# Optimization experiments

Measured on AMD Instinct MI355X. Metric: run time of the kernel, lower is better.

Reference implementation:

```python
import jax, jax.numpy as jnp
import numpy as np

NUM_FIELDS = 40
EMBED_DIM = 64
ATTN_DIM = 32

def _triu_index(n):
    i, j = np.triu_indices(n, k=1)
    return jnp.asarray(i, jnp.int32), jnp.asarray(j, jnp.int32)

def setup_inputs() -> dict:
    key = jax.random.key(0)
    k0, k1, k2, k3, k4, k5 = jax.random.split(key, 6)
    B = 8192
    inputs = jax.random.normal(k0, (B, NUM_FIELDS, EMBED_DIM), dtype=jnp.float32)
    # attention MLP params (PyTorch Linear default init scale ~ 1/sqrt(fan_in))
    s1 = 1.0 / np.sqrt(EMBED_DIM)
    s2 = 1.0 / np.sqrt(ATTN_DIM)
    W1 = jax.random.uniform(k1, (EMBED_DIM, ATTN_DIM), jnp.float32, -s1, s1)
    b1 = jax.random.uniform(k2, (ATTN_DIM,), jnp.float32, -s1, s1)
    w2 = jax.random.uniform(k3, (ATTN_DIM,), jnp.float32, -s2, s2)
    p = jax.random.uniform(k4, (EMBED_DIM,), jnp.float32, -s1, s1)
    return {"inputs": inputs, "W1": W1, "b1": b1, "w2": w2, "p": p}

def reference(inputs, W1, b1, w2, p):
    idx0, idx1 = _triu_index(NUM_FIELDS)  # [P], P = 780 pairs
    # gather pairwise field embeddings and take elementwise product: [B, P, D]
    prod = inputs[:, idx0, :] * inputs[:, idx1, :]
    # tiny attention MLP: Linear -> ReLU -> Linear(no bias) -> softmax over pairs
    h = jax.nn.relu(jnp.einsum('bpd,da->bpa', prod, W1) + b1)  # [B, P, A]
    logits = jnp.einsum('bpa,a->bp', h, w2)                    # [B, P]
    attn = jax.nn.softmax(logits, axis=1)                      # softmax over pair dim
    # attention-weighted sum pooling over pairs: [B, D]
    pooled = jnp.einsum('bp,bpd->bd', attn, prod)
    # final linear projection to scalar (dropout=0 / eval -> identity)
    return jnp.einsum('bd,d->b', pooled, p)
```

## Files before the change

kernel.cpp:

```cpp
#include <hip/hip_runtime.h>


typedef _Float16 f16;
typedef f16 f16x2 __attribute__((ext_vector_type(2)));
typedef f16 f16x8 __attribute__((ext_vector_type(8)));
typedef float fx16 __attribute__((ext_vector_type(16)));

#define NF 40
#define NB 8192

union V8 { f16x8 v8; f16x2 v2[4]; };

__global__ __launch_bounds__(256, 4) void afm_kernel(
    const float* __restrict__ x,
    const float* __restrict__ W1,
    const float* __restrict__ b1,
    const float* __restrict__ w2,
    const float* __restrict__ p,
    float* __restrict__ out)
{
    __shared__ f16 xh[4][NF * 64];

    const int wid  = threadIdx.x >> 6;
    const int lane = threadIdx.x & 63;
    const int b    = blockIdx.x * 4 + wid;
    f16* Xs = &xh[wid][0];

    const float4* xb = (const float4*)(x + (size_t)b * (NF * 64));
#pragma unroll
    for (int t = 0; t < 5; ++t) {
        int id = t * 64 + lane;
        float4 v0 = xb[id * 2];
        float4 v1 = xb[id * 2 + 1];
        f16x8 h = { (f16)v0.x, (f16)v0.y, (f16)v0.z, (f16)v0.w,
                    (f16)v1.x, (f16)v1.y, (f16)v1.z, (f16)v1.w };
        int row = id >> 3, g = id & 7;
        int blk = g ^ (row & 7);
        *(f16x8*)(Xs + (row << 6) + blk * 8) = h;
    }
    __syncthreads();

    const int nl = lane & 31;
    const int hh = lane >> 5;
    const int h8 = hh * 8;

    f16x8 w1f[4];
#pragma unroll
    for (int kt = 0; kt < 4; ++kt)
#pragma unroll
        for (int j = 0; j < 8; ++j)
            w1f[kt][j] = (f16)W1[(kt * 16 + h8 + j) * 32 + nl];

    f16x2 pp[16];
#pragma unroll
    for (int kt = 0; kt < 4; ++kt)
#pragma unroll
        for (int m = 0; m < 4; ++m) {
            f16x2 t2 = { (f16)p[kt * 16 + h8 + 2 * m], (f16)p[kt * 16 + h8 + 2 * m + 1] };
            pp[kt * 4 + m] = t2;
        }

    fx16 b1C;
    float w2v[16];
#pragma unroll
    for (int r = 0; r < 16; ++r) {
        int a = (r & 3) + 8 * (r >> 2) + 4 * hh;
        b1C[r] = b1[a];
        w2v[r] = w2[a];
    }

    f16x8 xif[4];
    {
        int rb = nl & 7;
        const f16* rowp = Xs + (nl << 6);
#pragma unroll
        for (int kt = 0; kt < 4; ++kt) {
            int blk = (kt * 2 + hh) ^ rb;
            xif[kt] = *(const f16x8*)(rowp + blk * 8);
        }
    }

    float accW = 0.f, accWS = 0.f;

    auto body = [&](const f16x8* xi, int jrow, bool masked, bool valid) {
        int rb = jrow & 7;
        const f16* rowp = Xs + (jrow << 6);
        V8 pr[4];
#pragma unroll
        for (int kt = 0; kt < 4; ++kt) {
            int blk = (kt * 2 + hh) ^ rb;
            f16x8 xj = *(const f16x8*)(rowp + blk * 8);
            pr[kt].v8 = xi[kt] * xj;
        }
        fx16 C = __builtin_amdgcn_mfma_f32_32x32x16_f16(w1f[0], pr[0].v8, b1C, 0, 0, 0);
        C = __builtin_amdgcn_mfma_f32_32x32x16_f16(w1f[1], pr[1].v8, C, 0, 0, 0);
        C = __builtin_amdgcn_mfma_f32_32x32x16_f16(w1f[2], pr[2].v8, C, 0, 0, 0);
        C = __builtin_amdgcn_mfma_f32_32x32x16_f16(w1f[3], pr[3].v8, C, 0, 0, 0);
        float sp = 0.f;
#pragma unroll
        for (int kt = 0; kt < 4; ++kt)
#pragma unroll
            for (int m = 0; m < 4; ++m)
                sp = __builtin_amdgcn_fdot2(pr[kt].v2[m], pp[kt * 4 + m], sp, false);
        float l0 = 0.f, l1 = 0.f;
#pragma unroll
        for (int r = 0; r < 8; ++r) {
            l0 = fmaf(fmaxf(C[2 * r], 0.f),     w2v[2 * r],     l0);
            l1 = fmaf(fmaxf(C[2 * r + 1], 0.f), w2v[2 * r + 1], l1);
        }
        float l = l0 + l1;
        l  += __shfl_xor(l, 32);
        sp += __shfl_xor(sp, 32);
        float w = __expf(l);
        if (masked && !valid) w = 0.f;
        accW += w;
        accWS = fmaf(w, sp, accWS);
    };

    for (int t = 1; t <= 15; ++t)
        body(xif, (nl + t) & 31, false, true);
    body(xif, (nl + 16) & 31, true, nl < 16);

    for (int u = 0; u < 8; ++u)
        body(xif, 32 + u, false, true);

    {
        int q = nl < 28 ? nl : 27;
        float disc = 225.0f - 8.0f * (float)q;
        int ii = (int)((15.0f - sqrtf(disc)) * 0.5f);
        if (ii * (15 - ii) / 2 > q) --ii;
        if ((ii + 1) * (14 - ii) / 2 <= q) ++ii;
        int jj = q - ii * (15 - ii) / 2 + ii + 1;
        int iC = 32 + ii, jC = 32 + jj;
        f16x8 xi2[4];
        int rb = iC & 7;
        const f16* rowp = Xs + (iC << 6);
#pragma unroll
        for (int kt = 0; kt < 4; ++kt) {
            int blk = (kt * 2 + hh) ^ rb;
            xi2[kt] = *(const f16x8*)(rowp + blk * 8);
        }
        body(xi2, jC, true, nl < 28);
    }

#pragma unroll
    for (int m = 16; m >= 1; m >>= 1) {
        accW  += __shfl_xor(accW, m);
        accWS += __shfl_xor(accWS, m);
    }
    if (lane == 0) out[b] = accWS / accW;
}

extern "C" void kernel_launch(void* const* d_in, const int* in_sizes, int n_in,
                              void* d_out, int out_size, void* d_ws, size_t ws_size,
                              hipStream_t stream) {
    const float* x  = (const float*)d_in[0];
    const float* W1 = (const float*)d_in[1];
    const float* b1 = (const float*)d_in[2];
    const float* w2 = (const float*)d_in[3];
    const float* p  = (const float*)d_in[4];
    float* out = (float*)d_out;
    dim3 grid(NB / 4), block(256);
    hipLaunchKernelGGL(afm_kernel, grid, block, 0, stream, x, W1, b1, w2, p, out);
}
```

Measured before the change: 158.3 us.

## Process two batch rows per wavefront and pack w2 epilogue into fp16 dot2

Result: slower. 209.4 us (+32.2%).

```diff
diff --git a/kernel.cpp b/kernel.cpp
--- a/kernel.cpp
+++ b/kernel.cpp
@@ -19,24 +19,29 @@
     const float* __restrict__ p,
     float* __restrict__ out)
 {
-    __shared__ f16 xh[4][NF * 64];
+    __shared__ f16 xh[8][NF * 64];
 
-    const int wid  = threadIdx.x >> 6;
-    const int lane = threadIdx.x & 63;
-    const int b    = blockIdx.x * 4 + wid;
-    f16* Xs = &xh[wid][0];
+    const int tid  = threadIdx.x;
+    const int wid  = tid >> 6;
+    const int lane = tid & 63;
+    const int b0   = blockIdx.x * 8 + wid * 2;
 
-    const float4* xb = (const float4*)(x + (size_t)b * (NF * 64));
+    f16* Xs0 = &xh[wid * 2][0];
+    f16* Xs1 = &xh[wid * 2 + 1][0];
+
+    const float4* xb = (const float4*)(x + (size_t)b0 * (NF * 64));
 #pragma unroll
-    for (int t = 0; t < 5; ++t) {
-        int id = t * 64 + lane;
-        float4 v0 = xb[id * 2];
-        float4 v1 = xb[id * 2 + 1];
+    for (int t = 0; t < 10; ++t) {
+        int g = t * 64 + lane;
+        float4 v0 = xb[g * 2];
+        float4 v1 = xb[g * 2 + 1];
         f16x8 h = { (f16)v0.x, (f16)v0.y, (f16)v0.z, (f16)v0.w,
                     (f16)v1.x, (f16)v1.y, (f16)v1.z, (f16)v1.w };
-        int row = id >> 3, g = id & 7;
-        int blk = g ^ (row & 7);
-        *(f16x8*)(Xs + (row << 6) + blk * 8) = h;
+        int bsel = (g >= 320);
+        int gi = g - (bsel ? 320 : 0);
+        int row = gi >> 3, gg = gi & 7;
+        int blk = gg ^ (row & 7);
+        *(f16x8*)((bsel ? Xs1 : Xs0) + (row << 6) + blk * 8) = h;
     }
     __syncthreads();
 
@@ -61,28 +66,37 @@
         }
 
     fx16 b1C;
-    float w2v[16];
+    f16x2 w2h[8];
 #pragma unroll
     for (int r = 0; r < 16; ++r) {
         int a = (r & 3) + 8 * (r >> 2) + 4 * hh;
         b1C[r] = b1[a];
-        w2v[r] = w2[a];
+    }
+#pragma unroll
+    for (int m = 0; m < 8; ++m) {
+        int r = 2 * m;
+        int a = (r & 3) + 8 * (r >> 2) + 4 * hh;
+        f16x2 t2 = { (f16)w2[a], (f16)w2[a + 1] };
+        w2h[m] = t2;
     }
 
-    f16x8 xif[4];
+    f16x8 xif0[4], xif1[4];
     {
         int rb = nl & 7;
-        const f16* rowp = Xs + (nl << 6);
+        const f16* r0 = Xs0 + (nl << 6);
+        const f16* r1 = Xs1 + (nl << 6);
 #pragma unroll
         for (int kt = 0; kt < 4; ++kt) {
             int blk = (kt * 2 + hh) ^ rb;
-            xif[kt] = *(const f16x8*)(rowp + blk * 8);
+            xif0[kt] = *(const f16x8*)(r0 + blk * 8);
+            xif1[kt] = *(const f16x8*)(r1 + blk * 8);
         }
     }
 
-    float accW = 0.f, accWS = 0.f;
+    float aW0 = 0.f, aS0 = 0.f, aW1 = 0.f, aS1 = 0.f;
 
-    auto body = [&](const f16x8* xi, int jrow, bool masked, bool valid) {
+    auto body = [&](const f16* Xs, const f16x8* xi, int jrow,
+                    float& aW, float& aS, bool valid) {
         int rb = jrow & 7;
         const f16* rowp = Xs + (jrow << 6);
         V8 pr[4];
@@ -96,33 +110,40 @@
         C = __builtin_amdgcn_mfma_f32_32x32x16_f16(w1f[1], pr[1].v8, C, 0, 0, 0);
         C = __builtin_amdgcn_mfma_f32_32x32x16_f16(w1f[2], pr[2].v8, C, 0, 0, 0);
         C = __builtin_amdgcn_mfma_f32_32x32x16_f16(w1f[3], pr[3].v8, C, 0, 0, 0);
-        float sp = 0.f;
+        float s0 = 0.f, s1 = 0.f, s2 = 0.f, s3 = 0.f;
 #pragma unroll
-        for (int kt = 0; kt < 4; ++kt)
-#pragma unroll
-            for (int m = 0; m < 4; ++m)
-                sp = __builtin_amdgcn_fdot2(pr[kt].v2[m], pp[kt * 4 + m], sp, false);
+        for (int m = 0; m < 4; ++m) {
+            s0 = __builtin_amdgcn_fdot2(pr[0].v2[m], pp[m],      s0, false);
+            s1 = __builtin_amdgcn_fdot2(pr[1].v2[m], pp[4 + m],  s1, false);
+            s2 = __builtin_amdgcn_fdot2(pr[2].v2[m], pp[8 + m],  s2, false);
+            s3 = __builtin_amdgcn_fdot2(pr[3].v2[m], pp[12 + m], s3, false);
+        }
+        float sp = (s0 + s1) + (s2 + s3);
+        const f16x2 z2 = { (f16)0.f, (f16)0.f };
         float l0 = 0.f, l1 = 0.f;
 #pragma unroll
-        for (int r = 0; r < 8; ++r) {
-            l0 = fmaf(fmaxf(C[2 * r], 0.f),     w2v[2 * r],     l0);
-            l1 = fmaf(fmaxf(C[2 * r + 1], 0.f), w2v[2 * r + 1], l1);
+        for (int m = 0; m < 8; ++m) {
+            f16x2 hm = __builtin_bit_cast(f16x2,
+                __builtin_amdgcn_cvt_pkrtz(C[2 * m], C[2 * m + 1]));
+            hm = __builtin_elementwise_max(hm, z2);
+            if (m & 1) l1 = __builtin_amdgcn_fdot2(hm, w2h[m], l1, false);
+            else       l0 = __builtin_amdgcn_fdot2(hm, w2h[m], l0, false);
         }
         float l = l0 + l1;
         l  += __shfl_xor(l, 32);
         sp += __shfl_xor(sp, 32);
         float w = __expf(l);
-        if (masked && !valid) w = 0.f;
-        accW += w;
-        accWS = fmaf(w, sp, accWS);
+        if (!valid) w = 0.f;
+        aW += w;
+        aS = fmaf(w, sp, aS);
     };
 
-    for (int t = 1; t <= 15; ++t)
-        body(xif, (nl + t) & 31, false, true);
-    body(xif, (nl + 16) & 31, true, nl < 16);
-
-    for (int u = 0; u < 8; ++u)
-        body(xif, 32 + u, false, true);
+    for (int t = 1; t <= 24; ++t) {
+        int jrow = (t <= 16) ? ((nl + t) & 31) : (t + 15);
+        bool valid = (t != 16) || (nl < 16);
+        body(Xs0, xif0, jrow, aW0, aS0, valid);
+        body(Xs1, xif1, jrow, aW1, aS1, valid);
+    }
 
     {
         int q = nl < 28 ? nl : 27;
@@ -132,23 +153,32 @@
         if ((ii + 1) * (14 - ii) / 2 <= q) ++ii;
         int jj = q - ii * (15 - ii) / 2 + ii + 1;
         int iC = 32 + ii, jC = 32 + jj;
+        bool vC = nl < 28;
+        int rb = iC & 7;
         f16x8 xi2[4];
-        int rb = iC & 7;
-        const f16* rowp = Xs + (iC << 6);
+        const f16* r0 = Xs0 + (iC << 6);
 #pragma unroll
-        for (int kt = 0; kt < 4; ++kt) {
-            int blk = (kt * 2 + hh) ^ rb;
-            xi2[kt] = *(const f16x8*)(rowp + blk * 8);
-        }
-        body(xi2, jC, true, nl < 28);
+        for (int kt = 0; kt < 4; ++kt)
+            xi2[kt] = *(const f16x8*)(r0 + (((kt * 2 + hh) ^ rb)) * 8);
+        body(Xs0, xi2, jC, aW0, aS0, vC);
+        const f16* r1 = Xs1 + (iC << 6);
+#pragma unroll
+        for (int kt = 0; kt < 4; ++kt)
+            xi2[kt] = *(const f16x8*)(r1 + (((kt * 2 + hh) ^ rb)) * 8);
+        body(Xs1, xi2, jC, aW1, aS1, vC);
     }
 
 #pragma unroll
     for (int m = 16; m >= 1; m >>= 1) {
-        accW  += __shfl_xor(accW, m);
-        accWS += __shfl_xor(accWS, m);
+        aW0 += __shfl_xor(aW0, m);
+        aS0 += __shfl_xor(aS0, m);
+        aW1 += __shfl_xor(aW1, m);
+        aS1 += __shfl_xor(aS1, m);
     }
-    if (lane == 0) out[b] = accWS / accW;
+    if (lane == 0) {
+        out[b0]     = aS0 / aW0;
+        out[b0 + 1] = aS1 / aW1;
+    }
 }
 
 extern "C" void kernel_launch(void* const* d_in, const int* in_sizes, int n_in,
@@ -160,6 +190,6 @@
     const float* w2 = (const float*)d_in[3];
     const float* p  = (const float*)d_in[4];
     float* out = (float*)d_out;
-    dim3 grid(NB / 4), block(256);
+    dim3 grid(NB / 8), block(256);
     hipLaunchKernelGGL(afm_kernel, grid, block, 0, stream, x, W1, b1, w2, p, out);
 }
```
